# Kernel optimization log

Hardware: AMD Instinct MI355X
Metric: run time of the kernel (lower is better)

## Reference

```python
import jax, jax.numpy as jnp
import numpy as np

ANGRES = 5  # u = v = angRes, n = 25


def _l2norm(x, axis):
    n = jnp.sqrt(jnp.sum(x * x, axis=axis, keepdims=True))
    return x / jnp.maximum(n, 1e-12)  # matches torch F.normalize eps


def _cos_attn(qm, km, vm):
    # qm: (b, M, K), km: (b, K, M), vm: (b, M, K)
    q = _l2norm(qm, -1)
    k = _l2norm(km, -2)
    att = jax.nn.softmax(q @ k, axis=-1)  # (b, M, M)
    return att @ vm


def _af_attn(x, u, v):  # AngularFrequencyAttention: b c (u v) h w -> b (c u) (h v w)
    b, c, n, h, w = x.shape
    t = x.reshape(b, c, u, v, h, w)
    qm = t.transpose(0, 1, 2, 4, 3, 5).reshape(b, c * u, h * v * w)   # (b,c,u,h,v,w)
    km = t.transpose(0, 4, 3, 5, 1, 2).reshape(b, h * v * w, c * u)   # (b,h,v,w,c,u)
    o = _cos_attn(qm, km, qm)
    o = o.reshape(b, c, u, h, v, w).transpose(0, 1, 2, 4, 3, 5).reshape(b, c, n, h, w)
    return o + x


def _sa_attn(x, u, v):  # SpatialAngularAttention: b c (u v) h w -> b (h u) (c v w)
    b, c, n, h, w = x.shape
    t = x.reshape(b, c, u, v, h, w)
    qm = t.transpose(0, 4, 2, 1, 3, 5).reshape(b, h * u, c * v * w)   # (b,h,u,c,v,w)
    km = t.transpose(0, 1, 3, 5, 4, 2).reshape(b, c * v * w, h * u)   # (b,c,v,w,h,u)
    o = _cos_attn(qm, km, qm)
    o = o.reshape(b, h, u, c, v, w).transpose(0, 3, 2, 4, 1, 5).reshape(b, c, n, h, w)
    return o + x


def _sf_attn(x, u, v):  # SpatialFrequencyAttention: b c (u v) h w -> b (c h) (w u v)
    b, c, n, h, w = x.shape
    t = x.reshape(b, c, u, v, h, w)
    qm = t.transpose(0, 1, 4, 5, 2, 3).reshape(b, c * h, w * u * v)   # (b,c,h,w,u,v)
    km = t.transpose(0, 5, 2, 3, 1, 4).reshape(b, w * u * v, c * h)   # (b,w,u,v,c,h)
    o = _cos_attn(qm, km, qm)
    o = o.reshape(b, c, h, w, u, v).transpose(0, 1, 4, 5, 2, 3).reshape(b, c, n, h, w)
    return o + x


def _layernorm(x, g, bta, eps=1e-5):
    mu = jnp.mean(x, -1, keepdims=True)
    var = jnp.mean(jnp.square(x - mu), -1, keepdims=True)
    return (x - mu) * jax.lax.rsqrt(var + eps) * g + bta


def setup_inputs() -> dict:
    key = jax.random.key(0)
    k0, k1, k2 = jax.random.split(key, 3)
    b, c, n, h, w = 4, 64, 25, 48, 48
    x = jax.random.normal(k0, (b, c, n, h, w), dtype=jnp.float32)
    gamma = jnp.ones((3 * c,), dtype=jnp.float32)
    beta = jnp.zeros((3 * c,), dtype=jnp.float32)
    w1 = jax.random.normal(k1, (3 * c, c), dtype=jnp.float32) * 0.02
    w2 = jax.random.normal(k2, (c, c), dtype=jnp.float32) * 0.02
    return {"x": x, "gamma": gamma, "beta": beta, "w1": w1, "w2": w2}


def reference(x, gamma, beta, w1, w2):
    u = v = ANGRES
    b, c, n, h, w = x.shape
    sf = _sf_attn(x, u, v)
    af = _af_attn(x, u, v)
    sa = _sa_attn(x, u, v)
    cat = jnp.concatenate([sf, af, sa], axis=1)            # (b, 3c, n, h, w)
    f = cat.transpose(0, 3, 4, 2, 1).reshape(b * h * w, n, 3 * c)
    y = _layernorm(f, gamma, beta)
    y = jax.nn.relu(y @ w1) @ w2                            # (bhw, n, c); dropout p=0.01 is eval-identity
    out = y.reshape(b, h, w, n, c).transpose(0, 4, 3, 1, 2) + x
    return out
```

## Files before the change

kernel.cpp:

```cpp
#include <hip/hip_runtime.h>
#include <stdint.h>

typedef __attribute__((ext_vector_type(8))) short bf16x8;
typedef __attribute__((ext_vector_type(4))) float f32x4;

__device__ __forceinline__ float b2f(short s) {
  union { unsigned u; float f; } a; a.u = ((unsigned)(unsigned short)s) << 16; return a.f;
}
__device__ __forceinline__ short f2b(float f) {
  union { float f; unsigned u; } a; a.f = f;
  unsigned r = a.u + 0x7fffu + ((a.u >> 16) & 1u);
  return (short)(r >> 16);
}
__device__ __forceinline__ void gload16(const void* g, void* l) {
  __builtin_amdgcn_global_load_lds((__attribute__((address_space(1))) void*)g,
                                   (__attribute__((address_space(3))) void*)l, 16, 0, 0);
}

#define SWZ(row, col) ((col) ^ (((row) & 7) << 3))


__global__ __launch_bounds__(256) void permute_sf_k(const float* __restrict__ x, short* __restrict__ Q) {
  __shared__ float buf[4][1200];
  int wave = threadIdx.x >> 6, lane = threadIdx.x & 63;
  int gr = blockIdx.x * 4 + wave;
  int b = gr / 3072, m = gr - b * 3072;
  int c = m / 48, hh = m - c * 48;
  const float* xb = x + (long)(b * 64 + c) * 57600 + hh * 48;
  for (int uv = 0; uv < 25; ++uv)
    if (lane < 48) buf[wave][uv * 48 + lane] = xb[uv * 2304 + lane];
  __syncthreads();
  short* Qr = Q + (long)gr * 1280;
  for (int k = lane; k < 1280; k += 64) {
    float v = 0.f;
    if (k < 1200) { int wv = k / 25, uv = k - wv * 25; v = buf[wave][uv * 48 + wv]; }
    Qr[k] = f2b(v);
  }
}

template<int BR>
__global__ __launch_bounds__(256) void permtr_k(const float* __restrict__ x,
                                                short* __restrict__ Q, short* __restrict__ QT) {
  constexpr int M  = (BR == 1) ? 320 : 240;
  constexpr int Mp = (BR == 1) ? 384 : 256;
  constexpr int Kp = (BR == 1) ? 11520 : 15360;
  __shared__ short t[32][33];
  int b = blockIdx.z;
  int k0 = blockIdx.x * 32, m0 = blockIdx.y * 32;
  int tx = threadIdx.x & 31, ty = threadIdx.x >> 5;
  const float* xb = x + (long)b * 3686400;
  #pragma unroll
  for (int i = 0; i < 32; i += 8) {
    int m = m0 + ty + i, k = k0 + tx;
    float v = 0.f;
    if (m < M) {
      int q1 = k / 240, r2 = k - q1 * 240;
      int v5 = r2 / 48, wv = r2 - v5 * 48;
      int a1 = m / 5, u = m - a1 * 5;
      long xi;
      if (BR == 1) xi = ((long)a1 * 25 + u * 5 + v5) * 2304 + q1 * 48 + wv;
      else         xi = ((long)q1 * 25 + u * 5 + v5) * 2304 + a1 * 48 + wv;
      v = xb[xi];
    }
    t[ty + i][tx] = f2b(v);
  }
  __syncthreads();
  long Qb = (long)b * Mp * Kp;
  #pragma unroll
  for (int i = 0; i < 32; i += 8)
    Q[Qb + (long)(m0 + ty + i) * Kp + k0 + tx] = t[ty + i][tx];
  #pragma unroll
  for (int i = 0; i < 32; i += 8)
    QT[Qb + (long)(k0 + ty + i) * Mp + m0 + tx] = t[tx][ty + i];
}

__global__ __launch_bounds__(256) void transpose_k(const short* __restrict__ in, short* __restrict__ out,
                                                   int R, int C) {
  __shared__ short t[32][33];
  long base = (long)blockIdx.z * R * C;
  int c0 = blockIdx.x * 32, r0 = blockIdx.y * 32;
  int tx = threadIdx.x & 31, ty = threadIdx.x >> 5;
  #pragma unroll
  for (int i = 0; i < 32; i += 8)
    t[ty + i][tx] = in[base + (long)(r0 + ty + i) * C + c0 + tx];
  __syncthreads();
  #pragma unroll
  for (int i = 0; i < 32; i += 8)
    out[base + (long)(c0 + ty + i) * R + r0 + tx] = t[tx][ty + i];
}

__global__ __launch_bounds__(256) void invnorm_k(const short* __restrict__ Q, long sQ, int Kp,
                                                 int Mvalid, int Mp, float* __restrict__ inv) {
  __shared__ float red[256];
  int m = blockIdx.x, b = blockIdx.y, tid = threadIdx.x;
  float acc = 0.f;
  if (m < Mvalid) {
    const short* row = Q + (long)b * sQ + (long)m * Kp;
    for (int k = tid * 8; k < Kp; k += 2048) {
      bf16x8 v = *(const bf16x8*)&row[k];
      #pragma unroll
      for (int j = 0; j < 8; ++j) { float f = b2f(v[j]); acc += f * f; }
    }
  }
  red[tid] = acc; __syncthreads();
  #pragma unroll
  for (int s2 = 128; s2 > 0; s2 >>= 1) {
    if (tid < s2) red[tid] += red[tid + s2];
    __syncthreads();
  }
  if (tid == 0)
    inv[(long)b * Mp + m] = (m < Mvalid) ? 1.0f / fmaxf(sqrtf(red[0]), 1e-12f) : 1.0f;
}

__global__ __launch_bounds__(256) void gemm1_tri_k(const short* __restrict__ Q,
                                                   const float* __restrict__ invn,
                                                   short* __restrict__ att) {
  __shared__ short sm[32768];
  int tid = threadIdx.x, wave = tid >> 6, lane = tid & 63;
  int la = lane & 15, lb = lane >> 4;
  int bat = blockIdx.z;
  int bx = blockIdx.x, yt = 0, rem = bx;
  while (rem >= 24 - yt) { rem -= 24 - yt; ++yt; }
  int xt = yt + rem;
  const short* Qb = Q + (long)bat * 3932160L;
  const float* inv = invn + (long)bat * 3072;
  int row0 = yt * 128, col0 = xt * 128;
  f32x4 acc[4][4] = {};
  int wr = wave >> 1, wc = wave & 1;
  int rloc = tid >> 3, cbase = (tid & 7) * 8;

  #define TRI_STAGE(KT, BUF) { \
    int k0 = (KT) * 64; \
    short* Asb = sm + (BUF) * 16384; \
    short* Bsb = Asb + 8192; \
    _Pragma("unroll") \
    for (int p = 0; p < 4; ++p) { \
      int row = p * 32 + rloc; \
      int sc = SWZ(row, cbase); \
      gload16(Qb + (long)(row0 + row) * 1280 + k0 + sc, (void*)(Asb + p * 2048 + tid * 8)); \
      gload16(Qb + (long)(col0 + row) * 1280 + k0 + sc, (void*)(Bsb + p * 2048 + tid * 8)); \
    } }
  #define TRI_COMP(BUF) { \
    const short* Asb = sm + (BUF) * 16384; \
    const short* Bsb = Asb + 8192; \
    _Pragma("unroll") \
    for (int kk = 0; kk < 64; kk += 32) { \
      bf16x8 av[4], bv[4]; \
      _Pragma("unroll") \
      for (int m = 0; m < 4; ++m) \
        av[m] = *(const bf16x8*)&Asb[(wr * 64 + m * 16 + la) * 64 + SWZ(la, kk + lb * 8)]; \
      _Pragma("unroll") \
      for (int nn = 0; nn < 4; ++nn) \
        bv[nn] = *(const bf16x8*)&Bsb[(wc * 64 + nn * 16 + la) * 64 + SWZ(la, kk + lb * 8)]; \
      _Pragma("unroll") \
      for (int m = 0; m < 4; ++m) \
        _Pragma("unroll") \
        for (int nn = 0; nn < 4; ++nn) \
          acc[m][nn] = __builtin_amdgcn_mfma_f32_16x16x32_bf16(av[m], bv[nn], acc[m][nn], 0, 0, 0); \
    } }

  TRI_STAGE(0, 0)
  for (int kt = 0; kt < 19; ++kt) {
    TRI_STAGE(kt + 1, (kt + 1) & 1)
    asm volatile("s_waitcnt vmcnt(8)" ::: "memory");
    __builtin_amdgcn_s_barrier();
    TRI_COMP(kt & 1)
    asm volatile("" ::: "memory");
    __builtin_amdgcn_s_barrier();
  }
  asm volatile("s_waitcnt vmcnt(0)" ::: "memory");
  __builtin_amdgcn_s_barrier();
  TRI_COMP(1)
  asm volatile("" ::: "memory");
  __builtin_amdgcn_s_barrier();

  short* staged = sm;
  #pragma unroll
  for (int m = 0; m < 4; ++m) {
    #pragma unroll
    for (int nn = 0; nn < 4; ++nn) {
      int cl = wc * 64 + nn * 16 + la;
      float ic = inv[col0 + cl];
      #pragma unroll
      for (int j = 0; j < 4; ++j) {
        int rl = wr * 64 + m * 16 + lb * 4 + j;
        staged[rl * 136 + cl] = f2b(acc[m][nn][j] * inv[row0 + rl] * ic);
      }
    }
  }
  __syncthreads();
  short* attb = att + (long)bat * 9437184L;
  {
    int r = tid >> 1, half = tid & 1;
    short* dst = attb + (long)(row0 + r) * 3072 + col0 + half * 64;
    const short* src = &staged[r * 136 + half * 64];
    #pragma unroll
    for (int q = 0; q < 8; ++q)
      *(bf16x8*)&dst[q * 8] = *(const bf16x8*)&src[q * 8];
  }
  if (xt != yt) {
    int c = tid >> 1, half = tid & 1;
    short* dst = attb + (long)(col0 + c) * 3072 + row0 + half * 64;
    #pragma unroll
    for (int q = 0; q < 8; ++q) {
      bf16x8 o;
      #pragma unroll
      for (int jj = 0; jj < 8; ++jj)
        o[jj] = staged[(half * 64 + q * 8 + jj) * 136 + c];
      *(bf16x8*)&dst[q * 8] = o;
    }
  }
}

__global__ __launch_bounds__(256) void gemm_s_k(
    const short* __restrict__ A, long sA, int lda,
    int ktotal, int ksper, int SK,
    float* __restrict__ Sf, long sS, int ldc)
{
  __shared__ short sm[32768];
  int tid = threadIdx.x;
  int wave = tid >> 6, lane = tid & 63;
  int la = lane & 15, lb = lane >> 4;
  int bz = blockIdx.z;
  int bat = bz / SK, kc = bz - bat * SK;
  int row0 = blockIdx.y * 128, col0 = blockIdx.x * 128;
  const short* Ab = A + (long)bat * sA;
  int kb = kc * ksper, ke = min(ktotal, kb + ksper);
  int L = ke - kb;
  f32x4 acc[4][4] = {};
  int wr = wave >> 1, wc = wave & 1;
  int rloc = tid >> 3, cbase = (tid & 7) * 8;

  #define GS_STAGE(KT, BUF) { \
    int k0 = (KT) * 64; \
    short* Asb = sm + (BUF) * 16384; \
    short* Bsb = Asb + 8192; \
    _Pragma("unroll") \
    for (int p = 0; p < 4; ++p) { \
      int row = p * 32 + rloc; \
      int sc = SWZ(row, cbase); \
      gload16(Ab + (long)(row0 + row) * lda + k0 + sc, (void*)(Asb + p * 2048 + tid * 8)); \
      gload16(Ab + (long)(col0 + row) * lda + k0 + sc, (void*)(Bsb + p * 2048 + tid * 8)); \
    } }
  #define GS_COMP(BUF) { \
    const short* Asb = sm + (BUF) * 16384; \
    const short* Bsb = Asb + 8192; \
    _Pragma("unroll") \
    for (int kk = 0; kk < 64; kk += 32) { \
      bf16x8 av[4], bv[4]; \
      _Pragma("unroll") \
      for (int m = 0; m < 4; ++m) \
        av[m] = *(const bf16x8*)&Asb[(wr * 64 + m * 16 + la) * 64 + SWZ(la, kk + lb * 8)]; \
      _Pragma("unroll") \
      for (int nn = 0; nn < 4; ++nn) \
        bv[nn] = *(const bf16x8*)&Bsb[(wc * 64 + nn * 16 + la) * 64 + SWZ(la, kk + lb * 8)]; \
      _Pragma("unroll") \
      for (int m = 0; m < 4; ++m) \
        _Pragma("unroll") \
        for (int nn = 0; nn < 4; ++nn) \
          acc[m][nn] = __builtin_amdgcn_mfma_f32_16x16x32_bf16(av[m], bv[nn], acc[m][nn], 0, 0, 0); \
    } }

  GS_STAGE(kb, 0)
  for (int t = 0; t < L - 1; ++t) {
    GS_STAGE(kb + t + 1, (t + 1) & 1)
    asm volatile("s_waitcnt vmcnt(8)" ::: "memory");
    __builtin_amdgcn_s_barrier();
    GS_COMP(t & 1)
    asm volatile("" ::: "memory");
    __builtin_amdgcn_s_barrier();
  }
  asm volatile("s_waitcnt vmcnt(0)" ::: "memory");
  __builtin_amdgcn_s_barrier();
  GS_COMP((L - 1) & 1)

  float* Sb = Sf + (long)bat * sS;
  #pragma unroll
  for (int m = 0; m < 4; ++m) {
    int gr0 = row0 + wr * 64 + m * 16 + lb * 4;
    #pragma unroll
    for (int nn = 0; nn < 4; ++nn) {
      int gc = col0 + wc * 64 + nn * 16 + la;
      #pragma unroll
      for (int j = 0; j < 4; ++j)
        atomicAdd(&Sb[(long)(gr0 + j) * ldc + gc], acc[m][nn][j]);
    }
  }
}

__global__ __launch_bounds__(256) void softmax_k(const float* __restrict__ Sf, long sS,
                                                 const float* __restrict__ inv,
                                                 int Mvalid, int Mp,
                                                 short* __restrict__ att, long sAtt) {
  __shared__ float srow[3072];
  __shared__ float red[256];
  int row = blockIdx.x, b = blockIdx.y, tid = threadIdx.x;
  const float* Sr = Sf + (long)b * sS + (long)row * Mp;
  const float* invb = inv + (long)b * Mp;
  float inv_i = invb[row];
  for (int j = tid; j < Mvalid; j += 256) srow[j] = Sr[j] * inv_i * invb[j];
  __syncthreads();
  float mx = -1e30f;
  for (int j = tid; j < Mvalid; j += 256) mx = fmaxf(mx, srow[j]);
  red[tid] = mx; __syncthreads();
  #pragma unroll
  for (int s2 = 128; s2 > 0; s2 >>= 1) {
    if (tid < s2) red[tid] = fmaxf(red[tid], red[tid + s2]);
    __syncthreads();
  }
  mx = red[0]; __syncthreads();
  float sum = 0.f;
  for (int j = tid; j < Mvalid; j += 256) {
    float e = __expf(srow[j] - mx);
    srow[j] = e; sum += e;
  }
  red[tid] = sum; __syncthreads();
  #pragma unroll
  for (int s2 = 128; s2 > 0; s2 >>= 1) {
    if (tid < s2) red[tid] += red[tid + s2];
    __syncthreads();
  }
  float rden = 1.0f / red[0];
  short* ar = att + (long)b * sAtt + (long)row * Mp;
  for (int j = tid; j < Mp; j += 256)
    ar[j] = (j < Mvalid) ? f2b(srow[j] * rden) : (short)0;
}

__global__ __launch_bounds__(256) void softmax_bf16_k(short* __restrict__ att, long sAtt, int M) {
  __shared__ float srow[3072];
  __shared__ float red[256];
  int row = blockIdx.x, b = blockIdx.y, tid = threadIdx.x;
  short* ar = att + (long)b * sAtt + (long)row * M;
  float mx = -1e30f;
  for (int j = tid * 8; j < M; j += 2048) {
    bf16x8 v = *(const bf16x8*)&ar[j];
    #pragma unroll
    for (int jj = 0; jj < 8; ++jj) { float f = b2f(v[jj]); srow[j + jj] = f; mx = fmaxf(mx, f); }
  }
  red[tid] = mx; __syncthreads();
  #pragma unroll
  for (int s2 = 128; s2 > 0; s2 >>= 1) {
    if (tid < s2) red[tid] = fmaxf(red[tid], red[tid + s2]);
    __syncthreads();
  }
  mx = red[0]; __syncthreads();
  float sum = 0.f;
  for (int j = tid; j < M; j += 256) {
    float e = __expf(srow[j] - mx);
    srow[j] = e; sum += e;
  }
  red[tid] = sum; __syncthreads();
  #pragma unroll
  for (int s2 = 128; s2 > 0; s2 >>= 1) {
    if (tid < s2) red[tid] += red[tid + s2];
    __syncthreads();
  }
  float rden = 1.0f / red[0];
  for (int j = tid * 8; j < M; j += 2048) {
    bf16x8 o;
    #pragma unroll
    for (int jj = 0; jj < 8; ++jj) o[jj] = f2b(srow[j + jj] * rden);
    *(bf16x8*)&ar[j] = o;
  }
}

__global__ __launch_bounds__(256) void gemm2sf_k(const short* __restrict__ A,
                                                 const short* __restrict__ B,
                                                 short* __restrict__ F) {
  __shared__ short sm[32768];
  int tid = threadIdx.x, wave = tid >> 6, lane = tid & 63;
  int la = lane & 15, lb = lane >> 4;
  int wr = wave >> 1, wc = wave & 1;
  int wk;
  { int xcd = blockIdx.x & 7, j = blockIdx.x >> 3; wk = xcd * 120 + j; }
  int yt = wk % 24, rem = wk / 24;
  int xt = rem % 10, bat = rem / 10;
  const short* Ab = A + (long)bat * 9437184L;
  const short* Bb = B + (long)bat * 3932160L;
  int rloc = tid >> 3, cbase = (tid & 7) * 8;
  f32x4 acc[4][4] = {};

  #define G2_STAGE(KT, BUF) { \
    int k0 = (KT) * 64; \
    short* Asb = sm + (BUF) * 16384; \
    short* Bsb = Asb + 8192; \
    _Pragma("unroll") \
    for (int p = 0; p < 4; ++p) { \
      int row = p * 32 + rloc; \
      int sc = SWZ(row, cbase); \
      int rga = (row & 63) * 48 + yt * 2 + (row >> 6); \
      gload16(Ab + (long)rga * 3072 + k0 + sc, (void*)(Asb + p * 2048 + tid * 8)); \
      int rgb = xt * 128 + row; \
      gload16(Bb + (long)rgb * 3072 + k0 + sc, (void*)(Bsb + p * 2048 + tid * 8)); \
    } }
  #define G2_COMP(BUF) { \
    const short* Asb = sm + (BUF) * 16384; \
    const short* Bsb = Asb + 8192; \
    _Pragma("unroll") \
    for (int kk = 0; kk < 64; kk += 32) { \
      bf16x8 av[4], bv[4]; \
      _Pragma("unroll") \
      for (int m = 0; m < 4; ++m) \
        av[m] = *(const bf16x8*)&Asb[(wr * 64 + m * 16 + la) * 64 + SWZ(la, kk + lb * 8)]; \
      _Pragma("unroll") \
      for (int nn = 0; nn < 4; ++nn) \
        bv[nn] = *(const bf16x8*)&Bsb[(wc * 64 + nn * 16 + la) * 64 + SWZ(la, kk + lb * 8)]; \
      _Pragma("unroll") \
      for (int m = 0; m < 4; ++m) \
        _Pragma("unroll") \
        for (int nn = 0; nn < 4; ++nn) \
          acc[m][nn] = __builtin_amdgcn_mfma_f32_16x16x32_bf16(av[m], bv[nn], acc[m][nn], 0, 0, 0); \
    } }

  G2_STAGE(0, 0)
  for (int kt = 0; kt < 47; ++kt) {
    G2_STAGE(kt + 1, (kt + 1) & 1)
    asm volatile("s_waitcnt vmcnt(8)" ::: "memory");
    __builtin_amdgcn_s_barrier();
    G2_COMP(kt & 1)
    asm volatile("" ::: "memory");
    __builtin_amdgcn_s_barrier();
  }
  asm volatile("s_waitcnt vmcnt(0)" ::: "memory");
  __builtin_amdgcn_s_barrier();
  G2_COMP(1)
  asm volatile("" ::: "memory");
  __builtin_amdgcn_s_barrier();

  short* staged = sm;
  #pragma unroll
  for (int m = 0; m < 4; ++m) {
    #pragma unroll
    for (int nn = 0; nn < 4; ++nn) {
      int cc = wc * 64 + nn * 16 + la;
      short4 o;
      o.x = f2b(acc[m][nn][0]); o.y = f2b(acc[m][nn][1]);
      o.z = f2b(acc[m][nn][2]); o.w = f2b(acc[m][nn][3]);
      *(short4*)&staged[(cc * 2 + wr) * 72 + m * 16 + lb * 4] = o;
    }
  }
  __syncthreads();
  #pragma unroll
  for (int rd = 0; rd < 8; ++rd) {
    int chunk = rd * 32 + (tid >> 3);
    int part = tid & 7;
    bf16x8 v = *(const bf16x8*)&staged[chunk * 72 + part * 8];
    int cc = chunk >> 1, sub = chunk & 1;
    int gc = xt * 128 + cc;
    if (gc < 1200) {
      int hh = yt * 2 + sub;
      int wv = gc / 25, nidx = gc - wv * 25;
      long base = (((long)(bat * 48 + hh) * 48 + wv) * 25 + nidx) * 192 + part * 8;
      *(bf16x8*)&F[base] = v;
    }
  }
}

template<int BR>
__global__ __launch_bounds__(256) void gemm2_k(const short* __restrict__ A,
                                               const short* __restrict__ B,
                                               short* __restrict__ F) {
  constexpr int NX  = (BR == 2) ? 45 : 60;
  constexpr int NY  = (BR == 2) ? 5 : 4;
  constexpr int NWG = NX * NY * 4;
  constexpr int LDA = (BR == 2) ? 384 : 256;
  constexpr long SA = (BR == 2) ? 147456L : 65536L;
  constexpr long SB = (BR == 2) ? 4423680L : 3932160L;
  constexpr int KST = (BR == 2) ? 6 : 4;

  __shared__ short sm[20480];
  short* As = sm;
  short* Bs = sm + 4096;
  int tid = threadIdx.x, wave = tid >> 6, lane = tid & 63;
  int la = lane & 15, lb = lane >> 4;

  int wk;
  { constexpr int q = NWG / 8, r = NWG % 8;
    int xcd = blockIdx.x & 7, j = blockIdx.x >> 3;
    wk = (xcd < r) ? xcd * (q + 1) + j : r * (q + 1) + (xcd - r) * q + j; }
  int yt = wk % NY, rem = wk / NY;
  int xt = rem % NX, bat = rem / NX;

  const short* Ab = A + (long)bat * SA;
  const short* Bb = B + (long)bat * SB;
  f32x4 acc[4][4] = {};
  int rloc = tid >> 3, cbase = (tid & 7) * 8;

  for (int kt = 0; kt < KST; ++kt) {
    int k0 = kt * 64;
    #pragma unroll
    for (int p = 0; p < 2; ++p) {
      int r = p * 32 + rloc;
      int sc = SWZ(r, cbase);
      int e = p * 2048 + tid * 8;
      int rowg = (BR == 2) ? (r * 5 + yt) : (yt * 64 + r);
      gload16(Ab + (long)rowg * LDA + k0 + sc, (void*)(As + e));
    }
    #pragma unroll
    for (int p = 0; p < 8; ++p) {
      int rb = p * 32 + rloc;
      int sc = SWZ(rb, cbase);
      int e = p * 2048 + tid * 8;
      int rowg;
      if (BR == 3) { int c = rb & 63, g = rb >> 6; rowg = c * 240 + xt * 4 + g; }
      else rowg = xt * 256 + rb;
      gload16(Bb + (long)rowg * LDA + k0 + sc, (void*)(Bs + e));
    }
    __syncthreads();
    #pragma unroll
    for (int kk = 0; kk < 64; kk += 32) {
      bf16x8 av[4], bv[4];
      #pragma unroll
      for (int m = 0; m < 4; ++m)
        av[m] = *(const bf16x8*)&As[(m * 16 + la) * 64 + SWZ(la, kk + lb * 8)];
      #pragma unroll
      for (int nn = 0; nn < 4; ++nn)
        bv[nn] = *(const bf16x8*)&Bs[(wave * 64 + nn * 16 + la) * 64 + SWZ(la, kk + lb * 8)];
      #pragma unroll
      for (int m = 0; m < 4; ++m)
        #pragma unroll
        for (int nn = 0; nn < 4; ++nn)
          acc[m][nn] = __builtin_amdgcn_mfma_f32_16x16x32_bf16(av[m], bv[nn], acc[m][nn], 0, 0, 0);
    }
    __syncthreads();
  }

  short* staged = sm;
  #pragma unroll
  for (int m = 0; m < 4; ++m) {
    #pragma unroll
    for (int nn = 0; nn < 4; ++nn) {
      if (BR == 3) {
        #pragma unroll
        for (int j = 0; j < 4; ++j)
          staged[((m * 16 + lb * 4 + j) * 4 + wave) * 72 + nn * 16 + la] = f2b(acc[m][nn][j]);
      } else {
        short4 o;
        o.x = f2b(acc[m][nn][0]); o.y = f2b(acc[m][nn][1]);
        o.z = f2b(acc[m][nn][2]); o.w = f2b(acc[m][nn][3]);
        *(short4*)&staged[(wave * 64 + nn * 16 + la) * 72 + m * 16 + lb * 4] = o;
      }
    }
  }
  __syncthreads();

  #pragma unroll
  for (int rd = 0; rd < 8; ++rd) {
    int chunk = rd * 32 + (tid >> 3);
    int part = tid & 7;
    bf16x8 v = *(const bf16x8*)&staged[chunk * 72 + part * 8];
    long base; bool ok = true;
    if (BR == 2) {
      int gc = xt * 256 + chunk;
      int hh = gc / 240, r2 = gc - hh * 240, v5 = r2 / 48, wv = r2 - v5 * 48;
      base = (((long)(bat * 48 + hh) * 48 + wv) * 25 + yt * 5 + v5) * 192 + 64 + part * 8;
    } else {
      int r = chunk >> 2, g = chunk & 3;
      int gr = yt * 64 + r; ok = (gr < 240);
      int hh = gr / 5, u = gr - hh * 5;
      int r2 = xt * 4 + g, v5 = r2 / 48, wv = r2 - v5 * 48;
      base = (((long)(bat * 48 + hh) * 48 + wv) * 25 + u * 5 + v5) * 192 + 128 + part * 8;
    }
    if (ok) *(bf16x8*)&F[base] = v;
  }
}

__global__ __launch_bounds__(256) void prep_w_k(const float* __restrict__ w1, const float* __restrict__ w2,
                                                short* __restrict__ w1t, short* __restrict__ w2t) {
  int idx = blockIdx.x * 256 + threadIdx.x;
  if (idx < 12288) {
    int i = idx / 64, j = idx - i * 64;
    w1t[j * 192 + i] = f2b(w1[idx]);
  } else if (idx < 16384) {
    int k = idx - 12288;
    int i = k / 64, j = k - i * 64;
    w2t[j * 64 + i] = f2b(w2[k]);
  }
}

__global__ __launch_bounds__(256) void ln_mlp_mfma_k(
    const short* __restrict__ F, const float* __restrict__ x,
    const float* __restrict__ gamma, const float* __restrict__ beta,
    const short* __restrict__ w1t, const short* __restrict__ w2t,
    float* __restrict__ out)
{
  int n = blockIdx.x, hh = blockIdx.y, b = blockIdx.z;
  __shared__ short A1[48 * 200];
  __shared__ short Y1[48 * 72];
  __shared__ float Y2[48 * 66];
  __shared__ float xs[64 * 49];
  int tid = threadIdx.x, wave = tid >> 6, lane = tid & 63;
  int la = lane & 15, lb = lane >> 4;
  long Fb0 = ((long)(b * 48 + hh) * 1200 + n) * 192;
  long xb = (long)b * 3686400 + (long)n * 2304 + hh * 48;

  {
    int ch = tid >> 2, qq = tid & 3;
    const float* xr = x + xb + (long)ch * 57600 + qq * 12;
    #pragma unroll
    for (int i = 0; i < 12; ++i) xs[ch * 49 + qq * 12 + i] = xr[i];
  }
  __syncthreads();

  float g0 = gamma[lane], g1 = gamma[lane + 64], g2 = gamma[lane + 128];
  float bt0 = beta[lane], bt1 = beta[lane + 64], bt2 = beta[lane + 128];
  for (int r = wave; r < 48; r += 4) {
    const short* Fr = F + Fb0 + (long)r * 4800;
    float xv = xs[lane * 49 + r];
    float v0 = b2f(Fr[lane]) + xv, v1 = b2f(Fr[lane + 64]) + xv, v2 = b2f(Fr[lane + 128]) + xv;
    float s = v0 + v1 + v2;
    #pragma unroll
    for (int o = 32; o >= 1; o >>= 1) s += __shfl_xor(s, o, 64);
    float mu = s * (1.f / 192.f);
    float d0 = v0 - mu, d1 = v1 - mu, d2 = v2 - mu;
    float q = d0 * d0 + d1 * d1 + d2 * d2;
    #pragma unroll
    for (int o = 32; o >= 1; o >>= 1) q += __shfl_xor(q, o, 64);
    float rs = rsqrtf(q * (1.f / 192.f) + 1e-5f);
    A1[r * 200 + lane]       = f2b(d0 * rs * g0 + bt0);
    A1[r * 200 + lane + 64]  = f2b(d1 * rs * g1 + bt1);
    A1[r * 200 + lane + 128] = f2b(d2 * rs * g2 + bt2);
  }
  __syncthreads();

  f32x4 acc1[3] = {};
  #pragma unroll
  for (int ks = 0; ks < 6; ++ks) {
    bf16x8 bv = *(const bf16x8*)&w1t[(wave * 16 + la) * 192 + ks * 32 + lb * 8];
    #pragma unroll
    for (int m = 0; m < 3; ++m) {
      bf16x8 av = *(const bf16x8*)&A1[(m * 16 + la) * 200 + ks * 32 + lb * 8];
      acc1[m] = __builtin_amdgcn_mfma_f32_16x16x32_bf16(av, bv, acc1[m], 0, 0, 0);
    }
  }
  #pragma unroll
  for (int m = 0; m < 3; ++m)
    #pragma unroll
    for (int j = 0; j < 4; ++j)
      Y1[(m * 16 + lb * 4 + j) * 72 + wave * 16 + la] = f2b(fmaxf(acc1[m][j], 0.f));
  __syncthreads();

  f32x4 acc2[3] = {};
  #pragma unroll
  for (int ks = 0; ks < 2; ++ks) {
    bf16x8 bv = *(const bf16x8*)&w2t[(wave * 16 + la) * 64 + ks * 32 + lb * 8];
    #pragma unroll
    for (int m = 0; m < 3; ++m) {
      bf16x8 av = *(const bf16x8*)&Y1[(m * 16 + la) * 72 + ks * 32 + lb * 8];
      acc2[m] = __builtin_amdgcn_mfma_f32_16x16x32_bf16(av, bv, acc2[m], 0, 0, 0);
    }
  }
  #pragma unroll
  for (int m = 0; m < 3; ++m)
    #pragma unroll
    for (int j = 0; j < 4; ++j)
      Y2[(m * 16 + lb * 4 + j) * 66 + wave * 16 + la] = acc2[m][j];
  __syncthreads();

  #pragma unroll
  for (int i = 0; i < 12; ++i) {
    int e = tid + 256 * i;
    int cc = e / 48, wv = e - cc * 48;
    out[xb + (long)cc * 57600 + wv] = Y2[wv * 66 + cc] + xs[cc * 49 + wv];
  }
}

extern "C" void kernel_launch(void* const* d_in, const int* in_sizes, int n_in,
                              void* d_out, int out_size, void* d_ws, size_t ws_size,
                              hipStream_t stream) {
  (void)in_sizes; (void)n_in; (void)out_size;
  const float* x     = (const float*)d_in[0];
  const float* gamma = (const float*)d_in[1];
  const float* beta  = (const float*)d_in[2];
  const float* w1    = (const float*)d_in[3];
  const float* w2    = (const float*)d_in[4];
  float* out = (float*)d_out;

  const size_t NEED = 237191168UL;
  if (ws_size < NEED) return;
  char* ws = (char*)d_ws;
  short* F     = (short*)(ws);
  short* att   = (short*)(ws + 88473600UL);
  short* Qbf   = (short*)(ws + 163971072UL);
  short* QbfT  = (short*)(ws + 199360512UL);
  float* Sf    = (float*)(ws + 234749952UL);
  float* invn  = (float*)(ws + 237109248UL);
  short* w1t   = (short*)(ws + 237158400UL);
  short* w2t   = (short*)(ws + 237182976UL);

  prep_w_k<<<64, 256, 0, stream>>>(w1, w2, w1t, w2t);

  permute_sf_k<<<3072, 256, 0, stream>>>(x, Qbf);
  transpose_k<<<dim3(40, 96, 4), 256, 0, stream>>>(Qbf, QbfT, 3072, 1280);
  invnorm_k<<<dim3(3072, 4), 256, 0, stream>>>(Qbf, 3932160L, 1280, 3072, 3072, invn);
  gemm1_tri_k<<<dim3(300, 1, 4), 256, 0, stream>>>(Qbf, invn, att);
  softmax_bf16_k<<<dim3(3072, 4), 256, 0, stream>>>(att, 9437184L, 3072);
  gemm2sf_k<<<dim3(960), 256, 0, stream>>>(att, QbfT, F);

  permtr_k<1><<<dim3(360, 12, 4), 256, 0, stream>>>(x, Qbf, QbfT);
  invnorm_k<<<dim3(384, 4), 256, 0, stream>>>(Qbf, 4423680L, 11520, 320, 384, invn);
  hipMemsetAsync(Sf, 0, (size_t)4 * 384 * 384 * 4, stream);
  gemm_s_k<<<dim3(3, 3, 32), 256, 0, stream>>>(Qbf, 4423680L, 11520, 180, 23, 8, Sf, 147456L, 384);
  softmax_k<<<dim3(320, 4), 256, 0, stream>>>(Sf, 147456L, invn, 320, 384, att, 147456L);
  gemm2_k<2><<<dim3(900), 256, 0, stream>>>(att, QbfT, F);

  permtr_k<2><<<dim3(480, 8, 4), 256, 0, stream>>>(x, Qbf, QbfT);
  invnorm_k<<<dim3(256, 4), 256, 0, stream>>>(Qbf, 3932160L, 15360, 240, 256, invn);
  hipMemsetAsync(Sf, 0, (size_t)4 * 256 * 256 * 4, stream);
  gemm_s_k<<<dim3(2, 2, 64), 256, 0, stream>>>(Qbf, 3932160L, 15360, 240, 15, 16, Sf, 65536L, 256);
  softmax_k<<<dim3(240, 4), 256, 0, stream>>>(Sf, 65536L, invn, 240, 256, att, 65536L);
  gemm2_k<3><<<dim3(960), 256, 0, stream>>>(att, QbfT, F);

  ln_mlp_mfma_k<<<dim3(25, 48, 4), 256, 0, stream>>>(F, x, gamma, beta, w1t, w2t, out);
}
```

Before: 568.8 us.

## Fuse softmax exp into QK GEMM epilogue and defer row normalization to AV GEMM

Because cosine-similarity logits lie in [-1,1], the softmax max-subtraction is dropped. exp is applied directly in the gemm1_tri epilogue, with row sums accumulated by atomics into a buffer, and gemm2sf divides by that row sum in its epilogue. This removes the separate softmax_bf16 pass over the 3072x3072 attention matrices, which read and wrote them again. The other softmax kernels likewise drop their max pass. The LN/MLP kernel now stages its F rows into shared memory with vectorized loads. Row sums are built from bf16-rounded values, and the atomics add contention.

```diff
diff --git a/kernel.cpp b/kernel.cpp
--- a/kernel.cpp
+++ b/kernel.cpp
@@ -114,7 +114,8 @@
 
 __global__ __launch_bounds__(256) void gemm1_tri_k(const short* __restrict__ Q,
                                                    const float* __restrict__ invn,
-                                                   short* __restrict__ att) {
+                                                   short* __restrict__ att,
+                                                   float* __restrict__ rowsum) {
   __shared__ short sm[32768];
   int tid = threadIdx.x, wave = tid >> 6, lane = tid & 63;
   int la = lane & 15, lb = lane >> 4;
@@ -184,31 +185,44 @@
       #pragma unroll
       for (int j = 0; j < 4; ++j) {
         int rl = wr * 64 + m * 16 + lb * 4 + j;
-        staged[rl * 136 + cl] = f2b(acc[m][nn][j] * inv[row0 + rl] * ic);
+        staged[rl * 136 + cl] = f2b(__expf(acc[m][nn][j] * inv[row0 + rl] * ic));
       }
     }
   }
   __syncthreads();
   short* attb = att + (long)bat * 9437184L;
+  float* rsb = rowsum + (long)bat * 3072;
   {
     int r = tid >> 1, half = tid & 1;
     short* dst = attb + (long)(row0 + r) * 3072 + col0 + half * 64;
     const short* src = &staged[r * 136 + half * 64];
-    #pragma unroll
-    for (int q = 0; q < 8; ++q)
-      *(bf16x8*)&dst[q * 8] = *(const bf16x8*)&src[q * 8];
+    float s = 0.f;
+    #pragma unroll
+    for (int q = 0; q < 8; ++q) {
+      bf16x8 v = *(const bf16x8*)&src[q * 8];
+      *(bf16x8*)&dst[q * 8] = v;
+      #pragma unroll
+      for (int jj = 0; jj < 8; ++jj) s += b2f(v[jj]);
+    }
+    s += __shfl_xor(s, 1, 64);
+    if (half == 0) atomicAdd(&rsb[row0 + r], s);
   }
   if (xt != yt) {
     int c = tid >> 1, half = tid & 1;
     short* dst = attb + (long)(col0 + c) * 3072 + row0 + half * 64;
+    float s = 0.f;
     #pragma unroll
     for (int q = 0; q < 8; ++q) {
       bf16x8 o;
       #pragma unroll
-      for (int jj = 0; jj < 8; ++jj)
+      for (int jj = 0; jj < 8; ++jj) {
         o[jj] = staged[(half * 64 + q * 8 + jj) * 136 + c];
+        s += b2f(o[jj]);
+      }
       *(bf16x8*)&dst[q * 8] = o;
     }
+    s += __shfl_xor(s, 1, 64);
+    if (half == 0) atomicAdd(&rsb[col0 + c], s);
   }
 }
 
@@ -298,20 +312,9 @@
   const float* Sr = Sf + (long)b * sS + (long)row * Mp;
   const float* invb = inv + (long)b * Mp;
   float inv_i = invb[row];
-  for (int j = tid; j < Mvalid; j += 256) srow[j] = Sr[j] * inv_i * invb[j];
-  __syncthreads();
-  float mx = -1e30f;
-  for (int j = tid; j < Mvalid; j += 256) mx = fmaxf(mx, srow[j]);
-  red[tid] = mx; __syncthreads();
-  #pragma unroll
-  for (int s2 = 128; s2 > 0; s2 >>= 1) {
-    if (tid < s2) red[tid] = fmaxf(red[tid], red[tid + s2]);
-    __syncthreads();
-  }
-  mx = red[0]; __syncthreads();
   float sum = 0.f;
   for (int j = tid; j < Mvalid; j += 256) {
-    float e = __expf(srow[j] - mx);
+    float e = __expf(Sr[j] * inv_i * invb[j]);
     srow[j] = e; sum += e;
   }
   red[tid] = sum; __syncthreads();
@@ -326,46 +329,9 @@
     ar[j] = (j < Mvalid) ? f2b(srow[j] * rden) : (short)0;
 }
 
-__global__ __launch_bounds__(256) void softmax_bf16_k(short* __restrict__ att, long sAtt, int M) {
-  __shared__ float srow[3072];
-  __shared__ float red[256];
-  int row = blockIdx.x, b = blockIdx.y, tid = threadIdx.x;
-  short* ar = att + (long)b * sAtt + (long)row * M;
-  float mx = -1e30f;
-  for (int j = tid * 8; j < M; j += 2048) {
-    bf16x8 v = *(const bf16x8*)&ar[j];
-    #pragma unroll
-    for (int jj = 0; jj < 8; ++jj) { float f = b2f(v[jj]); srow[j + jj] = f; mx = fmaxf(mx, f); }
-  }
-  red[tid] = mx; __syncthreads();
-  #pragma unroll
-  for (int s2 = 128; s2 > 0; s2 >>= 1) {
-    if (tid < s2) red[tid] = fmaxf(red[tid], red[tid + s2]);
-    __syncthreads();
-  }
-  mx = red[0]; __syncthreads();
-  float sum = 0.f;
-  for (int j = tid; j < M; j += 256) {
-    float e = __expf(srow[j] - mx);
-    srow[j] = e; sum += e;
-  }
-  red[tid] = sum; __syncthreads();
-  #pragma unroll
-  for (int s2 = 128; s2 > 0; s2 >>= 1) {
-    if (tid < s2) red[tid] += red[tid + s2];
-    __syncthreads();
-  }
-  float rden = 1.0f / red[0];
-  for (int j = tid * 8; j < M; j += 2048) {
-    bf16x8 o;
-    #pragma unroll
-    for (int jj = 0; jj < 8; ++jj) o[jj] = f2b(srow[j + jj] * rden);
-    *(bf16x8*)&ar[j] = o;
-  }
-}
-
 __global__ __launch_bounds__(256) void gemm2sf_k(const short* __restrict__ A,
                                                  const short* __restrict__ B,
+                                                 const float* __restrict__ rowsum,
                                                  short* __restrict__ F) {
   __shared__ short sm[32768];
   int tid = threadIdx.x, wave = tid >> 6, lane = tid & 63;
@@ -427,6 +393,14 @@
   asm volatile("" ::: "memory");
   __builtin_amdgcn_s_barrier();
 
+  const float* rsb = rowsum + (long)bat * 3072;
+  float rs[4][4];
+  #pragma unroll
+  for (int m = 0; m < 4; ++m)
+    #pragma unroll
+    for (int j = 0; j < 4; ++j)
+      rs[m][j] = 1.0f / rsb[(m * 16 + lb * 4 + j) * 48 + yt * 2 + wr];
+
   short* staged = sm;
   #pragma unroll
   for (int m = 0; m < 4; ++m) {
@@ -434,8 +408,8 @@
     for (int nn = 0; nn < 4; ++nn) {
       int cc = wc * 64 + nn * 16 + la;
       short4 o;
-      o.x = f2b(acc[m][nn][0]); o.y = f2b(acc[m][nn][1]);
-      o.z = f2b(acc[m][nn][2]); o.w = f2b(acc[m][nn][3]);
+      o.x = f2b(acc[m][nn][0] * rs[m][0]); o.y = f2b(acc[m][nn][1] * rs[m][1]);
+      o.z = f2b(acc[m][nn][2] * rs[m][2]); o.w = f2b(acc[m][nn][3] * rs[m][3]);
       *(short4*)&staged[(cc * 2 + wr) * 72 + m * 16 + lb * 4] = o;
     }
   }
@@ -586,14 +560,24 @@
 {
   int n = blockIdx.x, hh = blockIdx.y, b = blockIdx.z;
   __shared__ short A1[48 * 200];
-  __shared__ short Y1[48 * 72];
-  __shared__ float Y2[48 * 66];
   __shared__ float xs[64 * 49];
+  __shared__ __align__(16) char pool[19584];
+  short* Fs = (short*)pool;
+  short* Y1 = (short*)pool;
+  float* Y2 = (float*)(pool + 6912);
   int tid = threadIdx.x, wave = tid >> 6, lane = tid & 63;
   int la = lane & 15, lb = lane >> 4;
   long Fb0 = ((long)(b * 48 + hh) * 1200 + n) * 192;
   long xb = (long)b * 3686400 + (long)n * 2304 + hh * 48;
 
+  #pragma unroll
+  for (int it = 0; it < 5; ++it) {
+    int ci = tid + 256 * it;
+    if (ci < 1152) {
+      int r = ci / 24, q = ci - r * 24;
+      *(bf16x8*)&Fs[r * 192 + q * 8] = *(const bf16x8*)&F[Fb0 + (long)r * 4800 + q * 8];
+    }
+  }
   {
     int ch = tid >> 2, qq = tid & 3;
     const float* xr = x + xb + (long)ch * 57600 + qq * 12;
@@ -604,10 +588,13 @@
 
   float g0 = gamma[lane], g1 = gamma[lane + 64], g2 = gamma[lane + 128];
   float bt0 = beta[lane], bt1 = beta[lane + 64], bt2 = beta[lane + 128];
-  for (int r = wave; r < 48; r += 4) {
-    const short* Fr = F + Fb0 + (long)r * 4800;
+  #pragma unroll 4
+  for (int rr = 0; rr < 12; ++rr) {
+    int r = wave * 12 + rr;
     float xv = xs[lane * 49 + r];
-    float v0 = b2f(Fr[lane]) + xv, v1 = b2f(Fr[lane + 64]) + xv, v2 = b2f(Fr[lane + 128]) + xv;
+    float v0 = b2f(Fs[r * 192 + lane]) + xv;
+    float v1 = b2f(Fs[r * 192 + lane + 64]) + xv;
+    float v2 = b2f(Fs[r * 192 + lane + 128]) + xv;
     float s = v0 + v1 + v2;
     #pragma unroll
     for (int o = 32; o >= 1; o >>= 1) s += __shfl_xor(s, o, 64);
@@ -693,9 +680,9 @@
   permute_sf_k<<<3072, 256, 0, stream>>>(x, Qbf);
   transpose_k<<<dim3(40, 96, 4), 256, 0, stream>>>(Qbf, QbfT, 3072, 1280);
   invnorm_k<<<dim3(3072, 4), 256, 0, stream>>>(Qbf, 3932160L, 1280, 3072, 3072, invn);
-  gemm1_tri_k<<<dim3(300, 1, 4), 256, 0, stream>>>(Qbf, invn, att);
-  softmax_bf16_k<<<dim3(3072, 4), 256, 0, stream>>>(att, 9437184L, 3072);
-  gemm2sf_k<<<dim3(960), 256, 0, stream>>>(att, QbfT, F);
+  hipMemsetAsync(Sf, 0, 49152, stream);
+  gemm1_tri_k<<<dim3(300, 1, 4), 256, 0, stream>>>(Qbf, invn, att, Sf);
+  gemm2sf_k<<<dim3(960), 256, 0, stream>>>(att, QbfT, Sf, F);
 
   permtr_k<1><<<dim3(360, 12, 4), 256, 0, stream>>>(x, Qbf, QbfT);
   invnorm_k<<<dim3(384, 4), 256, 0, stream>>>(Qbf, 4423680L, 11520, 320, 384, invn);
```

After: 517.4 us. -9.0%, faster.
